# Performance work log

Measured on AMD Instinct MI355X. Metric: run time of the kernel, lower is better.

The kernel has to match this reference:

```python
import jax, jax.numpy as jnp
import numpy as np
from jax import lax

B, D, RANK, HID = 8192, 4096, 16, 24


def setup_inputs() -> dict:
    key = jax.random.key(0)
    ks = jax.random.split(key, 12)
    return {
        "grad": jax.random.normal(ks[0], (B, D), jnp.float32),
        "embed": jax.random.normal(ks[1], (B, D), jnp.float32),
        # LRLinear layer 0 (init='id' -> randn)
        "u0": jax.random.normal(ks[2], (D, RANK), jnp.float32),
        "v0": jax.random.normal(ks[3], (RANK, D), jnp.float32),
        "b0": jnp.zeros((D,), jnp.float32),
        # LRLinear layer 1
        "u1": jax.random.normal(ks[4], (D, RANK), jnp.float32),
        "v1": jax.random.normal(ks[5], (RANK, D), jnp.float32),
        "b1": jnp.zeros((D,), jnp.float32),
        # coeff MLP: Linear(D, HID) -> ReLU -> Linear(HID, 1) -> sigmoid
        "w1": jax.random.normal(ks[6], (HID, D), jnp.float32) * 0.02,
        "bw1": jnp.zeros((HID,), jnp.float32),
        "w2": jax.random.normal(ks[7], (1, HID), jnp.float32) * 0.02,
        "bw2": jnp.zeros((1,), jnp.float32),
    }


def _lr_layer(x, u, v, b):
    # (u @ (v @ x.T)).T + b, clamped at 0  ==  relu(x @ v.T @ u.T + b)
    return jnp.maximum((x @ v.T) @ u.T + b, 0.0)


def reference(grad, embed, u0, v0, b0, u1, v1, b1, w1, bw1, w2, bw2):
    grad_ = grad.reshape(-1, grad.shape[-1]).astype(jnp.float32)  # [B, D]
    k = grad_.shape[0]

    # Welford running mean / S over the batch, fused into one parallel
    # reduction (mathematically identical to the sequential update_counter).
    mean = jnp.mean(grad_, axis=0)                       # grad_mean [D]
    s = jnp.sum((grad_ - mean) ** 2, axis=0)             # grad_s    [D]
    std = jnp.sqrt(s / (k - 1))                          # grad_std  [D]
    mean = lax.stop_gradient(mean)
    std = lax.stop_gradient(std)

    # norm=True path
    x0 = (grad_ - mean) / (std + 1e-7)                   # [B, D]

    # IDMLP: low-rank relu chain
    x = _lr_layer(x0, u0, v0, b0)
    x = _lr_layer(x, u1, v1, b1)

    # choice == 0: per-row L2 renormalization to x0's row norms
    xn = jnp.sqrt(jnp.sum(x ** 2, axis=1)) + 1e-8        # [B]
    x0n = jnp.sqrt(jnp.sum(x0 ** 2, axis=1)) + 1e-8      # [B]
    x = x / xn[:, None] * x0n[:, None]

    # coeff MLP on embed
    h = jnp.maximum(embed @ w1.T + bw1, 0.0)             # [B, HID]
    coeff = jax.nn.sigmoid(h @ w2.T + bw2)               # [B, 1]

    out = (1.0 - coeff) * x + coeff * x0                 # [B, D]
    return out, coeff
```

## Files before the change

### kernel.cpp

```cpp
#include <hip/hip_runtime.h>
#include <math.h>

#define BN 8192
#define DD 4096
#define RK 16
#define HIDN 24
#define NCHUNK 128

#define OFF_T0T  0
#define OFF_T1T  (OFF_T0T + RK*BN)
#define OFF_HT   (OFF_T1T + RK*BN)
#define ZCOUNT   (OFF_HT + 32*BN)
#define OFF_PS   (ZCOUNT)
#define OFF_PQ   (OFF_PS + NCHUNK*DD)
#define OFF_V1T  (OFF_PQ + NCHUNK*DD)
#define OFF_MEAN (OFF_V1T + DD*RK)
#define OFF_INV  (OFF_MEAN + DD)

typedef __attribute__((ext_vector_type(8))) __bf16 bf16x8;
typedef __attribute__((ext_vector_type(4))) float f32x4;

__device__ inline void split8(const float* p, bf16x8& hi, bf16x8& lo) {
    float4 a = *(const float4*)p;
    float4 b = *(const float4*)(p + 4);
    float v[8] = {a.x, a.y, a.z, a.w, b.x, b.y, b.z, b.w};
#pragma unroll
    for (int j = 0; j < 8; ++j) {
        __bf16 h = (__bf16)v[j];
        hi[j] = h;
        lo[j] = (__bf16)(v[j] - (float)h);
    }
}

__global__ __launch_bounds__(256) void k1a(const float* __restrict__ g,
                                           float* __restrict__ ps,
                                           float* __restrict__ pq) {
    int ct = blockIdx.x & 3, rc = blockIdx.x >> 2;
    int col = ct * 1024 + threadIdx.x * 4;
    size_t base = (size_t)rc * 64 * DD + col;
    float4 s1 = make_float4(0.f, 0.f, 0.f, 0.f);
    float4 s2 = make_float4(0.f, 0.f, 0.f, 0.f);
#pragma unroll 8
    for (int i = 0; i < 64; ++i) {
        float4 v = *(const float4*)(g + base + (size_t)i * DD);
        s1.x += v.x; s1.y += v.y; s1.z += v.z; s1.w += v.w;
        s2.x = fmaf(v.x, v.x, s2.x);
        s2.y = fmaf(v.y, v.y, s2.y);
        s2.z = fmaf(v.z, v.z, s2.z);
        s2.w = fmaf(v.w, v.w, s2.w);
    }
    *(float4*)(ps + (size_t)rc * DD + col) = s1;
    *(float4*)(pq + (size_t)rc * DD + col) = s2;
}

__global__ __launch_bounds__(256) void k1bT(const float* __restrict__ ps,
                                            const float* __restrict__ pq,
                                            const float* __restrict__ v1,
                                            float* __restrict__ meanw,
                                            float* __restrict__ invw,
                                            float* __restrict__ v1T) {
    int d = blockIdx.x * 256 + threadIdx.x;
    float s1 = 0.f, s2 = 0.f;
#pragma unroll 8
    for (int i = 0; i < NCHUNK; ++i) {
        s1 += ps[i * DD + d];
        s2 += pq[i * DD + d];
    }
    float mean = s1 / (float)BN;
    float var = (s2 - s1 * s1 / (float)BN) / (float)(BN - 1);
    var = fmaxf(var, 0.f);
    meanw[d] = mean;
    invw[d] = 1.f / (sqrtf(var) + 1e-7f);
    float v[16];
#pragma unroll
    for (int s = 0; s < 16; ++s) v[s] = v1[(size_t)s * DD + d];
#pragma unroll
    for (int s = 0; s < 4; ++s)
        *(float4*)(v1T + (size_t)d * 16 + s * 4) =
            make_float4(v[4 * s], v[4 * s + 1], v[4 * s + 2], v[4 * s + 3]);
}

__global__ __launch_bounds__(256) void k2m(const float* __restrict__ grad,
                                           const float* __restrict__ meanw,
                                           const float* __restrict__ invw,
                                           const float* __restrict__ v0,
                                           float* __restrict__ T0T) {
    __shared__ float red[4][256];
    int tid = threadIdx.x;
    int wv = tid >> 6, l = tid & 63;
    int lr = l & 15, lk = l >> 4;
    int m0 = (blockIdx.x >> 2) * 16;
    int kbase = (blockIdx.x & 3) * 1024 + wv * 256;
    const float* g0 = grad + (size_t)(m0 + lr) * DD + kbase + lk * 8;
    const float* vp = v0 + (size_t)lr * DD + kbase + lk * 8;
    const float* mp = meanw + kbase + lk * 8;
    const float* ip = invw + kbase + lk * 8;
    f32x4 acc = {0.f, 0.f, 0.f, 0.f};
#pragma unroll 2
    for (int ks = 0; ks < 8; ++ks) {
        int k0 = ks * 32;
        bf16x8 vhi, vlo;
        split8(vp + k0, vhi, vlo);
        float4 ma = *(const float4*)(mp + k0);
        float4 mb = *(const float4*)(mp + k0 + 4);
        float4 ia = *(const float4*)(ip + k0);
        float4 ib = *(const float4*)(ip + k0 + 4);
        float mv[8] = {ma.x, ma.y, ma.z, ma.w, mb.x, mb.y, mb.z, mb.w};
        float iv[8] = {ia.x, ia.y, ia.z, ia.w, ib.x, ib.y, ib.z, ib.w};
        float4 ga = *(const float4*)(g0 + k0);
        float4 gb = *(const float4*)(g0 + k0 + 4);
        float gv[8] = {ga.x, ga.y, ga.z, ga.w, gb.x, gb.y, gb.z, gb.w};
        bf16x8 xhi, xlo;
#pragma unroll
        for (int j = 0; j < 8; ++j) {
            float x = (gv[j] - mv[j]) * iv[j];
            __bf16 h = (__bf16)x;
            xhi[j] = h;
            xlo[j] = (__bf16)(x - (float)h);
        }
        acc = __builtin_amdgcn_mfma_f32_16x16x32_bf16(vhi, xhi, acc, 0, 0, 0);
        acc = __builtin_amdgcn_mfma_f32_16x16x32_bf16(vhi, xlo, acc, 0, 0, 0);
        acc = __builtin_amdgcn_mfma_f32_16x16x32_bf16(vlo, xhi, acc, 0, 0, 0);
    }
#pragma unroll
    for (int r = 0; r < 4; ++r)
        red[wv][(lk * 4 + r) * 16 + lr] = acc[r];
    __syncthreads();
    float s = red[0][tid] + red[1][tid] + red[2][tid] + red[3][tid];
    atomicAdd(&T0T[(size_t)(tid >> 4) * BN + m0 + (tid & 15)], s);
}

__global__ __launch_bounds__(256) void k3(const float* __restrict__ T0T,
                                          const float* __restrict__ u0,
                                          const float* __restrict__ b0,
                                          const float* __restrict__ v1T,
                                          float* __restrict__ T1T) {
    int b = (blockIdx.x >> 5) * 256 + threadIdx.x;
    int d0 = (blockIdx.x & 31) * 128;
    float t0[16];
#pragma unroll
    for (int r = 0; r < 16; ++r) t0[r] = T0T[(size_t)r * BN + b];
    float acc[16];
#pragma unroll
    for (int s = 0; s < 16; ++s) acc[s] = 0.f;
#pragma unroll 2
    for (int d = d0; d < d0 + 128; ++d) {
        const float* ur = u0 + (size_t)d * RK;
        float x1 = b0[d];
#pragma unroll
        for (int r = 0; r < 16; ++r) x1 = fmaf(ur[r], t0[r], x1);
        x1 = fmaxf(x1, 0.f);
        const float* vr = v1T + (size_t)d * RK;
#pragma unroll
        for (int s = 0; s < 16; ++s) acc[s] = fmaf(vr[s], x1, acc[s]);
    }
#pragma unroll
    for (int s = 0; s < 16; ++s)
        atomicAdd(&T1T[(size_t)s * BN + b], acc[s]);
}

__global__ __launch_bounds__(256) void k5m(const float* __restrict__ embed,
                                           const float* __restrict__ w1,
                                           float* __restrict__ HT) {
    __shared__ float red[4][512];
    int tid = threadIdx.x;
    int wv = tid >> 6, l = tid & 63;
    int lr = l & 15, lk = l >> 4;
    int m0 = (blockIdx.x >> 2) * 16;
    int kbase = (blockIdx.x & 3) * 1024 + wv * 256;
    int wr1 = (lr + 16 > 23) ? 23 : lr + 16;
    const float* e0 = embed + (size_t)(m0 + lr) * DD + kbase + lk * 8;
    const float* w0a = w1 + (size_t)lr * DD + kbase + lk * 8;
    const float* w0b = w1 + (size_t)wr1 * DD + kbase + lk * 8;
    f32x4 acc0 = {0.f, 0.f, 0.f, 0.f};
    f32x4 acc1 = {0.f, 0.f, 0.f, 0.f};
#pragma unroll 2
    for (int ks = 0; ks < 8; ++ks) {
        int k0 = ks * 32;
        bf16x8 whi0, wlo0, whi1, wlo1, ehi, elo;
        split8(w0a + k0, whi0, wlo0);
        split8(w0b + k0, whi1, wlo1);
        split8(e0 + k0, ehi, elo);
        acc0 = __builtin_amdgcn_mfma_f32_16x16x32_bf16(whi0, ehi, acc0, 0, 0, 0);
        acc1 = __builtin_amdgcn_mfma_f32_16x16x32_bf16(whi1, ehi, acc1, 0, 0, 0);
        acc0 = __builtin_amdgcn_mfma_f32_16x16x32_bf16(whi0, elo, acc0, 0, 0, 0);
        acc1 = __builtin_amdgcn_mfma_f32_16x16x32_bf16(whi1, elo, acc1, 0, 0, 0);
        acc0 = __builtin_amdgcn_mfma_f32_16x16x32_bf16(wlo0, ehi, acc0, 0, 0, 0);
        acc1 = __builtin_amdgcn_mfma_f32_16x16x32_bf16(wlo1, ehi, acc1, 0, 0, 0);
    }
#pragma unroll
    for (int r = 0; r < 4; ++r) {
        red[wv][(lk * 4 + r) * 16 + lr] = acc0[r];
        red[wv][256 + (lk * 4 + r) * 16 + lr] = acc1[r];
    }
    __syncthreads();
#pragma unroll
    for (int j = 0; j < 2; ++j) {
        int idx = tid + j * 256;
        float s = red[0][idx] + red[1][idx] + red[2][idx] + red[3][idx];
        int nt = idx >> 8, nr = (idx >> 4) & 15, cc = idx & 15;
        atomicAdd(&HT[(size_t)(nt * 16 + nr) * BN + m0 + cc], s);
    }
}

__device__ inline float dotu(const float4* ur, const float* t, float b) {
    float a = b;
#pragma unroll
    for (int rr = 0; rr < 4; ++rr) {
        a = fmaf(ur[rr].x, t[4 * rr + 0], a);
        a = fmaf(ur[rr].y, t[4 * rr + 1], a);
        a = fmaf(ur[rr].z, t[4 * rr + 2], a);
        a = fmaf(ur[rr].w, t[4 * rr + 3], a);
    }
    return a;
}

__global__ __launch_bounds__(1024) void k6fc(const float* __restrict__ grad,
                                             const float* __restrict__ meanw,
                                             const float* __restrict__ invw,
                                             const float* __restrict__ T1T,
                                             const float* __restrict__ u1,
                                             const float* __restrict__ b1,
                                             const float* __restrict__ HT,
                                             const float* __restrict__ bw1,
                                             const float* __restrict__ w2,
                                             const float* __restrict__ bw2,
                                             float* __restrict__ out) {
    __shared__ float redn[2][16];
    __shared__ float bc[2];
    __shared__ float cfs[16];
    int tid = threadIdx.x;
    int wv = tid >> 6, l = tid & 63;
    int row0 = blockIdx.x * 16;
    int c = tid * 4;

    if (tid < 16) {
        int b = row0 + tid;
        float z = bw2[0];
#pragma unroll
        for (int j = 0; j < HIDN; ++j) {
            float h = fmaxf(HT[(size_t)j * BN + b] + bw1[j], 0.f);
            z = fmaf(w2[j], h, z);
        }
        float cf = 1.f / (1.f + expf(-z));
        cfs[tid] = cf;
        out[(size_t)BN * DD + b] = cf;
    }

    float4 u[4][4];
#pragma unroll
    for (int cc = 0; cc < 4; ++cc)
#pragma unroll
        for (int rr = 0; rr < 4; ++rr)
            u[cc][rr] = *(const float4*)(u1 + (size_t)(c + cc) * RK + rr * 4);
    float4 bv = *(const float4*)(b1 + c);
    float4 mv = *(const float4*)(meanw + c);
    float4 iv = *(const float4*)(invw + c);
    __syncthreads();

    for (int row = 0; row < 16; ++row) {
        int b = row0 + row;
        float t[16];
#pragma unroll
        for (int r = 0; r < 16; ++r) t[r] = T1T[(size_t)r * BN + b];
        float4 g = *(const float4*)(grad + (size_t)b * DD + c);
        float4 x0;
        x0.x = (g.x - mv.x) * iv.x;
        x0.y = (g.y - mv.y) * iv.y;
        x0.z = (g.z - mv.z) * iv.z;
        x0.w = (g.w - mv.w) * iv.w;
        float4 x2;
        x2.x = fmaxf(dotu(u[0], t, bv.x), 0.f);
        x2.y = fmaxf(dotu(u[1], t, bv.y), 0.f);
        x2.z = fmaxf(dotu(u[2], t, bv.z), 0.f);
        x2.w = fmaxf(dotu(u[3], t, bv.w), 0.f);
        float s0 = x0.x * x0.x + x0.y * x0.y + x0.z * x0.z + x0.w * x0.w;
        float s2 = x2.x * x2.x + x2.y * x2.y + x2.z * x2.z + x2.w * x2.w;
#pragma unroll
        for (int off = 1; off < 64; off <<= 1) {
            s0 += __shfl_xor(s0, off);
            s2 += __shfl_xor(s2, off);
        }
        if (l == 0) {
            redn[0][wv] = s2;
            redn[1][wv] = s0;
        }
        __syncthreads();
        if (tid < 16) {
            float a2 = redn[0][tid], a0 = redn[1][tid];
#pragma unroll
            for (int off = 1; off < 16; off <<= 1) {
                a2 += __shfl_xor(a2, off);
                a0 += __shfl_xor(a0, off);
            }
            if (tid == 0) {
                float xn = sqrtf(a2) + 1e-8f;
                float x0n = sqrtf(a0) + 1e-8f;
                float cf = cfs[row];
                bc[0] = (1.f - cf) * x0n / xn;
                bc[1] = cf;
            }
        }
        __syncthreads();
        float s1 = bc[0], cf = bc[1];
        float4 o;
        o.x = fmaf(s1, x2.x, cf * x0.x);
        o.y = fmaf(s1, x2.y, cf * x0.y);
        o.z = fmaf(s1, x2.z, cf * x0.z);
        o.w = fmaf(s1, x2.w, cf * x0.w);
        *(float4*)(out + (size_t)b * DD + c) = o;
    }
}

extern "C" void kernel_launch(void* const* d_in, const int* in_sizes, int n_in,
                              void* d_out, int out_size, void* d_ws, size_t ws_size,
                              hipStream_t stream) {
    const float* grad = (const float*)d_in[0];
    const float* embed = (const float*)d_in[1];
    const float* u0 = (const float*)d_in[2];
    const float* v0 = (const float*)d_in[3];
    const float* b0 = (const float*)d_in[4];
    const float* u1 = (const float*)d_in[5];
    const float* v1 = (const float*)d_in[6];
    const float* b1 = (const float*)d_in[7];
    const float* w1 = (const float*)d_in[8];
    const float* bw1 = (const float*)d_in[9];
    const float* w2 = (const float*)d_in[10];
    const float* bw2 = (const float*)d_in[11];
    float* out = (float*)d_out;
    float* ws = (float*)d_ws;

    hipMemsetAsync(ws, 0, (size_t)ZCOUNT * sizeof(float), stream);

    k5m<<<2048, 256, 0, stream>>>(embed, w1, ws + OFF_HT);
    k1a<<<512, 256, 0, stream>>>(grad, ws + OFF_PS, ws + OFF_PQ);
    k1bT<<<16, 256, 0, stream>>>(ws + OFF_PS, ws + OFF_PQ, v1,
                                 ws + OFF_MEAN, ws + OFF_INV, ws + OFF_V1T);
    k2m<<<2048, 256, 0, stream>>>(grad, ws + OFF_MEAN, ws + OFF_INV, v0, ws + OFF_T0T);
    k3<<<1024, 256, 0, stream>>>(ws + OFF_T0T, u0, b0, ws + OFF_V1T, ws + OFF_T1T);
    k6fc<<<512, 1024, 0, stream>>>(grad, ws + OFF_MEAN, ws + OFF_INV, ws + OFF_T1T,
                                   u1, b1, ws + OFF_HT, bw1, w2, bw2, out);
}
```

Baseline: 491.6 us.

## Fold normalization into v0 weights and replace atomics with partial-sum buffers

Rewrites the first low-rank projection algebraically. v0 is pre-scaled by inv-std and pre-split into bf16 hi/lo in k1bT, and the term mean·v0' is subtracted as a per-rank constant, so k2m runs MFMA directly on raw grad. W1 is also pre-split once into bf16 hi/lo. All atomicAdd accumulations (T0T, T1T, HT) become plain stores into per-partition buffers that later stages reduce, which removes the large memset and atomic traffic. It adds an extra reduction kernel and more workspace traffic, and it risks cancellation error when the constant is subtracted for columns with large mean/std ratios.

Result: slower. 507.7 us (+3.3%).

```diff
diff --git a/kernel.cpp b/kernel.cpp
--- a/kernel.cpp
+++ b/kernel.cpp
@@ -7,15 +7,20 @@
 #define HIDN 24
 #define NCHUNK 128
 
-#define OFF_T0T  0
-#define OFF_T1T  (OFF_T0T + RK*BN)
-#define OFF_HT   (OFF_T1T + RK*BN)
-#define ZCOUNT   (OFF_HT + 32*BN)
-#define OFF_PS   (ZCOUNT)
+#define OFF_T0TP 0
+#define OFF_T1TP (OFF_T0TP + 4*RK*BN)
+#define OFF_HTP  (OFF_T1TP + 32*RK*BN)
+#define OFF_T1T  (OFF_HTP + 4*32*BN)
+#define OFF_PS   (OFF_T1T + RK*BN)
 #define OFF_PQ   (OFF_PS + NCHUNK*DD)
 #define OFF_V1T  (OFF_PQ + NCHUNK*DD)
 #define OFF_MEAN (OFF_V1T + DD*RK)
 #define OFF_INV  (OFF_MEAN + DD)
+#define OFF_C    (OFF_INV + DD)
+#define OFF_V0PH (OFF_C + 16)
+#define OFF_V0PL (OFF_V0PH + RK*DD/2)
+#define OFF_W1H  (OFF_V0PL + RK*DD/2)
+#define OFF_W1L  (OFF_W1H + HIDN*DD/2)
 
 typedef __attribute__((ext_vector_type(8))) __bf16 bf16x8;
 typedef __attribute__((ext_vector_type(4))) float f32x4;
@@ -29,6 +34,20 @@
         __bf16 h = (__bf16)v[j];
         hi[j] = h;
         lo[j] = (__bf16)(v[j] - (float)h);
+    }
+}
+
+__global__ __launch_bounds__(256) void k0w(const float* __restrict__ w1,
+                                           __bf16* __restrict__ w1h,
+                                           __bf16* __restrict__ w1l) {
+    int i = (blockIdx.x * 256 + threadIdx.x) * 4;
+    float4 v = *(const float4*)(w1 + i);
+    float vv[4] = {v.x, v.y, v.z, v.w};
+#pragma unroll
+    for (int j = 0; j < 4; ++j) {
+        __bf16 h = (__bf16)vv[j];
+        w1h[i + j] = h;
+        w1l[i + j] = (__bf16)(vv[j] - (float)h);
     }
 }
 
@@ -56,10 +75,18 @@
 __global__ __launch_bounds__(256) void k1bT(const float* __restrict__ ps,
                                             const float* __restrict__ pq,
                                             const float* __restrict__ v1,
+                                            const float* __restrict__ v0,
                                             float* __restrict__ meanw,
                                             float* __restrict__ invw,
-                                            float* __restrict__ v1T) {
-    int d = blockIdx.x * 256 + threadIdx.x;
+                                            float* __restrict__ v1T,
+                                            __bf16* __restrict__ v0ph,
+                                            __bf16* __restrict__ v0pl,
+                                            float* __restrict__ cvec) {
+    __shared__ float csum[16];
+    int tid = threadIdx.x;
+    int d = blockIdx.x * 256 + tid;
+    if (tid < 16) csum[tid] = 0.f;
+    __syncthreads();
     float s1 = 0.f, s2 = 0.f;
 #pragma unroll 8
     for (int i = 0; i < NCHUNK; ++i) {
@@ -69,8 +96,9 @@
     float mean = s1 / (float)BN;
     float var = (s2 - s1 * s1 / (float)BN) / (float)(BN - 1);
     var = fmaxf(var, 0.f);
+    float invv = 1.f / (sqrtf(var) + 1e-7f);
     meanw[d] = mean;
-    invw[d] = 1.f / (sqrtf(var) + 1e-7f);
+    invw[d] = invv;
     float v[16];
 #pragma unroll
     for (int s = 0; s < 16; ++s) v[s] = v1[(size_t)s * DD + d];
@@ -78,68 +106,75 @@
     for (int s = 0; s < 4; ++s)
         *(float4*)(v1T + (size_t)d * 16 + s * 4) =
             make_float4(v[4 * s], v[4 * s + 1], v[4 * s + 2], v[4 * s + 3]);
+    float pc[16];
+#pragma unroll
+    for (int r = 0; r < 16; ++r) {
+        float vp = v0[(size_t)r * DD + d] * invv;
+        __bf16 h = (__bf16)vp;
+        v0ph[(size_t)r * DD + d] = h;
+        v0pl[(size_t)r * DD + d] = (__bf16)(vp - (float)h);
+        pc[r] = vp * mean;
+    }
+#pragma unroll
+    for (int r = 0; r < 16; ++r) {
+        float x = pc[r];
+#pragma unroll
+        for (int off = 1; off < 64; off <<= 1) x += __shfl_xor(x, off);
+        if ((tid & 63) == 0) atomicAdd(&csum[r], x);
+    }
+    __syncthreads();
+    if (tid < 16) atomicAdd(&cvec[tid], csum[tid]);
 }
 
 __global__ __launch_bounds__(256) void k2m(const float* __restrict__ grad,
-                                           const float* __restrict__ meanw,
-                                           const float* __restrict__ invw,
-                                           const float* __restrict__ v0,
-                                           float* __restrict__ T0T) {
+                                           const __bf16* __restrict__ v0ph,
+                                           const __bf16* __restrict__ v0pl,
+                                           float* __restrict__ T0Tp) {
     __shared__ float red[4][256];
     int tid = threadIdx.x;
     int wv = tid >> 6, l = tid & 63;
     int lr = l & 15, lk = l >> 4;
     int m0 = (blockIdx.x >> 2) * 16;
-    int kbase = (blockIdx.x & 3) * 1024 + wv * 256;
+    int q = blockIdx.x & 3;
+    int kbase = q * 1024 + wv * 256;
     const float* g0 = grad + (size_t)(m0 + lr) * DD + kbase + lk * 8;
-    const float* vp = v0 + (size_t)lr * DD + kbase + lk * 8;
-    const float* mp = meanw + kbase + lk * 8;
-    const float* ip = invw + kbase + lk * 8;
+    const __bf16* vph = v0ph + (size_t)lr * DD + kbase + lk * 8;
+    const __bf16* vpl = v0pl + (size_t)lr * DD + kbase + lk * 8;
     f32x4 acc = {0.f, 0.f, 0.f, 0.f};
 #pragma unroll 2
     for (int ks = 0; ks < 8; ++ks) {
         int k0 = ks * 32;
-        bf16x8 vhi, vlo;
-        split8(vp + k0, vhi, vlo);
-        float4 ma = *(const float4*)(mp + k0);
-        float4 mb = *(const float4*)(mp + k0 + 4);
-        float4 ia = *(const float4*)(ip + k0);
-        float4 ib = *(const float4*)(ip + k0 + 4);
-        float mv[8] = {ma.x, ma.y, ma.z, ma.w, mb.x, mb.y, mb.z, mb.w};
-        float iv[8] = {ia.x, ia.y, ia.z, ia.w, ib.x, ib.y, ib.z, ib.w};
-        float4 ga = *(const float4*)(g0 + k0);
-        float4 gb = *(const float4*)(g0 + k0 + 4);
-        float gv[8] = {ga.x, ga.y, ga.z, ga.w, gb.x, gb.y, gb.z, gb.w};
-        bf16x8 xhi, xlo;
-#pragma unroll
-        for (int j = 0; j < 8; ++j) {
-            float x = (gv[j] - mv[j]) * iv[j];
-            __bf16 h = (__bf16)x;
-            xhi[j] = h;
-            xlo[j] = (__bf16)(x - (float)h);
-        }
-        acc = __builtin_amdgcn_mfma_f32_16x16x32_bf16(vhi, xhi, acc, 0, 0, 0);
-        acc = __builtin_amdgcn_mfma_f32_16x16x32_bf16(vhi, xlo, acc, 0, 0, 0);
-        acc = __builtin_amdgcn_mfma_f32_16x16x32_bf16(vlo, xhi, acc, 0, 0, 0);
+        bf16x8 vhi = *(const bf16x8*)(vph + k0);
+        bf16x8 vlo = *(const bf16x8*)(vpl + k0);
+        bf16x8 ghi, glo;
+        split8(g0 + k0, ghi, glo);
+        acc = __builtin_amdgcn_mfma_f32_16x16x32_bf16(vhi, ghi, acc, 0, 0, 0);
+        acc = __builtin_amdgcn_mfma_f32_16x16x32_bf16(vhi, glo, acc, 0, 0, 0);
+        acc = __builtin_amdgcn_mfma_f32_16x16x32_bf16(vlo, ghi, acc, 0, 0, 0);
     }
 #pragma unroll
     for (int r = 0; r < 4; ++r)
         red[wv][(lk * 4 + r) * 16 + lr] = acc[r];
     __syncthreads();
     float s = red[0][tid] + red[1][tid] + red[2][tid] + red[3][tid];
-    atomicAdd(&T0T[(size_t)(tid >> 4) * BN + m0 + (tid & 15)], s);
-}
-
-__global__ __launch_bounds__(256) void k3(const float* __restrict__ T0T,
+    T0Tp[(size_t)(q * 16 + (tid >> 4)) * BN + m0 + (tid & 15)] = s;
+}
+
+__global__ __launch_bounds__(256) void k3(const float* __restrict__ T0Tp,
+                                          const float* __restrict__ cvec,
                                           const float* __restrict__ u0,
                                           const float* __restrict__ b0,
                                           const float* __restrict__ v1T,
-                                          float* __restrict__ T1T) {
+                                          float* __restrict__ T1Tp) {
     int b = (blockIdx.x >> 5) * 256 + threadIdx.x;
-    int d0 = (blockIdx.x & 31) * 128;
+    int dt = blockIdx.x & 31;
+    int d0 = dt * 128;
     float t0[16];
 #pragma unroll
-    for (int r = 0; r < 16; ++r) t0[r] = T0T[(size_t)r * BN + b];
+    for (int r = 0; r < 16; ++r)
+        t0[r] = T0Tp[(size_t)r * BN + b] + T0Tp[(size_t)(16 + r) * BN + b] +
+                T0Tp[(size_t)(32 + r) * BN + b] + T0Tp[(size_t)(48 + r) * BN + b] -
+                cvec[r];
     float acc[16];
 #pragma unroll
     for (int s = 0; s < 16; ++s) acc[s] = 0.f;
@@ -156,30 +191,46 @@
     }
 #pragma unroll
     for (int s = 0; s < 16; ++s)
-        atomicAdd(&T1T[(size_t)s * BN + b], acc[s]);
+        T1Tp[(size_t)(dt * 16 + s) * BN + b] = acc[s];
+}
+
+__global__ __launch_bounds__(256) void k3r(const float* __restrict__ T1Tp,
+                                           float* __restrict__ T1T) {
+    int idx = blockIdx.x * 256 + threadIdx.x;
+    int r = idx >> 13, b = idx & 8191;
+    float s = 0.f;
+#pragma unroll 8
+    for (int p = 0; p < 32; ++p) s += T1Tp[(size_t)(p * 16 + r) * BN + b];
+    T1T[(size_t)r * BN + b] = s;
 }
 
 __global__ __launch_bounds__(256) void k5m(const float* __restrict__ embed,
-                                           const float* __restrict__ w1,
-                                           float* __restrict__ HT) {
+                                           const __bf16* __restrict__ w1h,
+                                           const __bf16* __restrict__ w1l,
+                                           float* __restrict__ HTp) {
     __shared__ float red[4][512];
     int tid = threadIdx.x;
     int wv = tid >> 6, l = tid & 63;
     int lr = l & 15, lk = l >> 4;
     int m0 = (blockIdx.x >> 2) * 16;
-    int kbase = (blockIdx.x & 3) * 1024 + wv * 256;
+    int q = blockIdx.x & 3;
+    int kbase = q * 1024 + wv * 256;
     int wr1 = (lr + 16 > 23) ? 23 : lr + 16;
     const float* e0 = embed + (size_t)(m0 + lr) * DD + kbase + lk * 8;
-    const float* w0a = w1 + (size_t)lr * DD + kbase + lk * 8;
-    const float* w0b = w1 + (size_t)wr1 * DD + kbase + lk * 8;
+    const __bf16* wha = w1h + (size_t)lr * DD + kbase + lk * 8;
+    const __bf16* wla = w1l + (size_t)lr * DD + kbase + lk * 8;
+    const __bf16* whb = w1h + (size_t)wr1 * DD + kbase + lk * 8;
+    const __bf16* wlb = w1l + (size_t)wr1 * DD + kbase + lk * 8;
     f32x4 acc0 = {0.f, 0.f, 0.f, 0.f};
     f32x4 acc1 = {0.f, 0.f, 0.f, 0.f};
 #pragma unroll 2
     for (int ks = 0; ks < 8; ++ks) {
         int k0 = ks * 32;
-        bf16x8 whi0, wlo0, whi1, wlo1, ehi, elo;
-        split8(w0a + k0, whi0, wlo0);
-        split8(w0b + k0, whi1, wlo1);
+        bf16x8 whi0 = *(const bf16x8*)(wha + k0);
+        bf16x8 wlo0 = *(const bf16x8*)(wla + k0);
+        bf16x8 whi1 = *(const bf16x8*)(whb + k0);
+        bf16x8 wlo1 = *(const bf16x8*)(wlb + k0);
+        bf16x8 ehi, elo;
         split8(e0 + k0, ehi, elo);
         acc0 = __builtin_amdgcn_mfma_f32_16x16x32_bf16(whi0, ehi, acc0, 0, 0, 0);
         acc1 = __builtin_amdgcn_mfma_f32_16x16x32_bf16(whi1, ehi, acc1, 0, 0, 0);
@@ -199,7 +250,7 @@
         int idx = tid + j * 256;
         float s = red[0][idx] + red[1][idx] + red[2][idx] + red[3][idx];
         int nt = idx >> 8, nr = (idx >> 4) & 15, cc = idx & 15;
-        atomicAdd(&HT[(size_t)(nt * 16 + nr) * BN + m0 + cc], s);
+        HTp[(size_t)(q * 32 + nt * 16 + nr) * BN + m0 + cc] = s;
     }
 }
 
@@ -221,7 +272,7 @@
                                              const float* __restrict__ T1T,
                                              const float* __restrict__ u1,
                                              const float* __restrict__ b1,
-                                             const float* __restrict__ HT,
+                                             const float* __restrict__ HTp,
                                              const float* __restrict__ bw1,
                                              const float* __restrict__ w2,
                                              const float* __restrict__ bw2,
@@ -239,7 +290,10 @@
         float z = bw2[0];
 #pragma unroll
         for (int j = 0; j < HIDN; ++j) {
-            float h = fmaxf(HT[(size_t)j * BN + b] + bw1[j], 0.f);
+            float h = HTp[(size_t)j * BN + b] + HTp[(size_t)(32 + j) * BN + b] +
+                      HTp[(size_t)(64 + j) * BN + b] + HTp[(size_t)(96 + j) * BN + b] +
+                      bw1[j];
+            h = fmaxf(h, 0.f);
             z = fmaf(w2[j], h, z);
         }
         float cf = 1.f / (1.f + expf(-z));
@@ -329,15 +383,23 @@
     const float* bw2 = (const float*)d_in[11];
     float* out = (float*)d_out;
     float* ws = (float*)d_ws;
-
-    hipMemsetAsync(ws, 0, (size_t)ZCOUNT * sizeof(float), stream);
-
-    k5m<<<2048, 256, 0, stream>>>(embed, w1, ws + OFF_HT);
+    __bf16* v0ph = (__bf16*)(ws + OFF_V0PH);
+    __bf16* v0pl = (__bf16*)(ws + OFF_V0PL);
+    __bf16* w1h = (__bf16*)(ws + OFF_W1H);
+    __bf16* w1l = (__bf16*)(ws + OFF_W1L);
+
+    hipMemsetAsync(ws + OFF_C, 0, 16 * sizeof(float), stream);
+
+    k0w<<<96, 256, 0, stream>>>(w1, w1h, w1l);
+    k5m<<<2048, 256, 0, stream>>>(embed, w1h, w1l, ws + OFF_HTP);
     k1a<<<512, 256, 0, stream>>>(grad, ws + OFF_PS, ws + OFF_PQ);
-    k1bT<<<16, 256, 0, stream>>>(ws + OFF_PS, ws + OFF_PQ, v1,
-                                 ws + OFF_MEAN, ws + OFF_INV, ws + OFF_V1T);
-    k2m<<<2048, 256, 0, stream>>>(grad, ws + OFF_MEAN, ws + OFF_INV, v0, ws + OFF_T0T);
-    k3<<<1024, 256, 0, stream>>>(ws + OFF_T0T, u0, b0, ws + OFF_V1T, ws + OFF_T1T);
+    k1bT<<<16, 256, 0, stream>>>(ws + OFF_PS, ws + OFF_PQ, v1, v0,
+                                 ws + OFF_MEAN, ws + OFF_INV, ws + OFF_V1T,
+                                 v0ph, v0pl, ws + OFF_C);
+    k2m<<<2048, 256, 0, stream>>>(grad, v0ph, v0pl, ws + OFF_T0TP);
+    k3<<<1024, 256, 0, stream>>>(ws + OFF_T0TP, ws + OFF_C, u0, b0,
+                                 ws + OFF_V1T, ws + OFF_T1TP);
+    k3r<<<512, 256, 0, stream>>>(ws + OFF_T1TP, ws + OFF_T1T);
     k6fc<<<512, 1024, 0, stream>>>(grad, ws + OFF_MEAN, ws + OFF_INV, ws + OFF_T1T,
-                                   u1, b1, ws + OFF_HT, bw1, w2, bw2, out);
-}
+                                   u1, b1, ws + OFF_HTP, bw1, w2, bw2, out);
+}
```
